# Optimization experiments

Measured on AMD Instinct MI355X. Metric: run time of the kernel, lower is better.

The kernel has to match this reference:

```python
import jax, jax.numpy as jnp
import numpy as np
import math

B, S, D, H, DK, DFF = 64, 512, 512, 8, 64, 2048


def _layernorm(x, g, b, eps=1e-5):
    mu = jnp.mean(x, axis=-1, keepdims=True)
    var = jnp.var(x, axis=-1, keepdims=True)
    return (x - mu) * jax.lax.rsqrt(var + eps) * g + b


def setup_inputs() -> dict:
    key = jax.random.key(0)
    ks = jax.random.split(key, 16)
    std = 0.02
    return {
        "query": jax.random.normal(ks[0], (B, S, D), jnp.float32),
        "key": jax.random.normal(ks[1], (B, S, D), jnp.float32),
        "values": jax.random.normal(ks[2], (B, S, D), jnp.float32),
        "forget_rate": jax.random.uniform(ks[3], (B, 1, S, 1), jnp.float32),
        "Wq": jax.random.normal(ks[4], (D, D), jnp.float32) * std,
        "bq": jnp.zeros((D,), jnp.float32),
        "Wk": jax.random.normal(ks[5], (D, D), jnp.float32) * std,
        "bk": jnp.zeros((D,), jnp.float32),
        "Wv": jax.random.normal(ks[6], (D, D), jnp.float32) * std,
        "bv": jnp.zeros((D,), jnp.float32),
        "Wo": jax.random.normal(ks[7], (D, D), jnp.float32) * std,
        "bo": jnp.zeros((D,), jnp.float32),
        "g1": jnp.ones((D,), jnp.float32),
        "beta1": jnp.zeros((D,), jnp.float32),
        "W1": jax.random.normal(ks[8], (D, DFF), jnp.float32) * std,
        "bf1": jnp.zeros((DFF,), jnp.float32),
        "W2": jax.random.normal(ks[9], (DFF, D), jnp.float32) * std,
        "bf2": jnp.zeros((D,), jnp.float32),
        "g2": jnp.ones((D,), jnp.float32),
        "beta2": jnp.zeros((D,), jnp.float32),
        "mask": 0,
    }


def reference(query, key, values, forget_rate, Wq, bq, Wk, bk, Wv, bv, Wo, bo,
              g1, beta1, W1, bf1, W2, bf2, g2, beta2, mask):
    bs, seqlen, _ = query.shape
    # project and split heads -> [B, H, S, DK]
    q = (query @ Wq + bq).reshape(bs, seqlen, H, DK).transpose(0, 2, 1, 3)
    k = (key @ Wk + bk).reshape(bs, seqlen, H, DK).transpose(0, 2, 1, 3)
    v = (values @ Wv + bv).reshape(bs, seqlen, H, DK).transpose(0, 2, 1, 3)

    scores = jnp.einsum('bhqd,bhkd->bhqk', q, k) / math.sqrt(DK)  # [B,H,S,S]
    # forget_rate [B,1,S,1] broadcasts over heads and key dim (== repeat in torch)
    scores = scores * forget_rate
    # src_mask: allowed where triu(ones, k=mask) == 0, i.e. j < i + mask
    allowed = jnp.tril(jnp.ones((seqlen, seqlen), bool), mask - 1)
    scores = jnp.where(allowed, scores, jnp.float32(-1e32))
    probs = jax.nn.softmax(scores, axis=-1)
    if mask == 0:  # zero_pad: overwrite first query row with zeros
        probs = probs.at[:, :, 0, :].set(0.0)
    out = jnp.einsum('bhqk,bhkd->bhqd', probs, v)  # [B,H,S,DK]
    concat = out.transpose(0, 2, 1, 3).reshape(bs, seqlen, D)
    attn_out = concat @ Wo + bo

    x = _layernorm(query + attn_out, g1, beta1)
    ff = jax.nn.relu(x @ W1 + bf1) @ W2 + bf2
    x = _layernorm(x + ff, g2, beta2)
    return x
```

## Files before the change

kernel.cpp:

```cpp
#include <hip/hip_runtime.h>
#include <hip/hip_bf16.h>
#include <stdint.h>

typedef __attribute__((ext_vector_type(8))) short short8;
typedef __attribute__((ext_vector_type(8))) unsigned short ushort8;
typedef __attribute__((ext_vector_type(4))) unsigned short ushort4v;
typedef __attribute__((ext_vector_type(4))) float f32x4;

#define DEV static __device__ __forceinline__

constexpr int Bc = 64, Sc = 512, Dc = 512, Hc = 8, DKc = 64, DFc = 2048;
constexpr int Mtot = Bc * Sc;
constexpr int CB   = 16;
constexpr int RC   = CB * Sc;

DEV unsigned short f2b(float f) {
    union { float f; unsigned u; } x; x.f = f;
    unsigned r = x.u + 0x7fffu + ((x.u >> 16) & 1u);
    return (unsigned short)(r >> 16);
}
DEV float b2f(unsigned short u) {
    union { unsigned u; float f; } x; x.u = ((unsigned)u) << 16; return x.f;
}

DEV void gload16(const void* g, void* l) {
    __builtin_amdgcn_global_load_lds(
        (const __attribute__((address_space(1))) void*)g,
        (__attribute__((address_space(3))) void*)l, 16, 0, 0);
}

__global__ void k_cvt(const float* __restrict__ in, unsigned short* __restrict__ out, int n8) {
    int idx = blockIdx.x * 256 + threadIdx.x;
    if (idx >= n8) return;
    const float4* p = (const float4*)(in + (size_t)idx * 8);
    float4 a = p[0], b = p[1];
    ushort8 o;
    o[0] = f2b(a.x); o[1] = f2b(a.y); o[2] = f2b(a.z); o[3] = f2b(a.w);
    o[4] = f2b(b.x); o[5] = f2b(b.y); o[6] = f2b(b.z); o[7] = f2b(b.w);
    *(ushort8*)(out + (size_t)idx * 8) = o;
}

__global__ void k_copy8(const unsigned short* __restrict__ in, unsigned short* __restrict__ out, int n8) {
    int idx = blockIdx.x * 256 + threadIdx.x;
    if (idx >= n8) return;
    *(ushort8*)(out + (size_t)idx * 8) = *(const ushort8*)(in + (size_t)idx * 8);
}

__global__ void k_cvt_w_all(
    const float* __restrict__ Wq, const float* __restrict__ Wk, const float* __restrict__ Wv,
    const float* __restrict__ Wo, const float* __restrict__ W1, const float* __restrict__ W2,
    unsigned short* __restrict__ Wqt, unsigned short* __restrict__ Wkt,
    unsigned short* __restrict__ Wvt, unsigned short* __restrict__ Wot,
    unsigned short* __restrict__ W1t, unsigned short* __restrict__ W2t) {
    int idx = blockIdx.x * 256 + threadIdx.x;
    const float* in; unsigned short* out; int K, N, li;
    if (idx < 131072) {
        int w = idx >> 15, r = idx & 32767;
        const float* ins[4] = {Wq, Wk, Wv, Wo};
        unsigned short* outs[4] = {Wqt, Wkt, Wvt, Wot};
        in = ins[w]; out = outs[w]; K = 512; N = 512; li = r;
    } else if (idx < 262144) {
        in = W1; out = W1t; K = 512; N = 2048; li = idx - 131072;
    } else {
        in = W2; out = W2t; K = 2048; N = 512; li = idx - 262144;
    }
    int kc = li % (K / 8), n = li / (K / 8);
    ushort8 o;
    #pragma unroll
    for (int j = 0; j < 8; ++j) o[j] = f2b(in[(size_t)(kc * 8 + j) * N + n]);
    *(ushort8*)(out + (size_t)n * K + kc * 8) = o;
}

__global__ void k_cvt_all(
    const float* __restrict__ Wq, const float* __restrict__ Wk, const float* __restrict__ Wv,
    const float* __restrict__ Wo, const float* __restrict__ W1, const float* __restrict__ W2,
    unsigned short* __restrict__ Wqt, unsigned short* __restrict__ Wkt,
    unsigned short* __restrict__ Wvt, unsigned short* __restrict__ Wot,
    unsigned short* __restrict__ W1t, unsigned short* __restrict__ W2t,
    const float* __restrict__ q_in, const float* __restrict__ k_in, const float* __restrict__ v_in,
    unsigned short* __restrict__ q_out, unsigned short* __restrict__ k_out,
    unsigned short* __restrict__ v_out) {
    int idx = blockIdx.x * 256 + threadIdx.x;
    if (idx >= 393216) {
        int a = idx - 393216;
        const float* in; unsigned short* out; int li;
        if (a < 2097152)       { in = q_in; out = q_out; li = a; }
        else if (a < 4194304)  { in = k_in; out = k_out; li = a - 2097152; }
        else                   { in = v_in; out = v_out; li = a - 4194304; }
        const float4* p = (const float4*)(in + (size_t)li * 8);
        float4 x = p[0], y = p[1];
        ushort8 o;
        o[0] = f2b(x.x); o[1] = f2b(x.y); o[2] = f2b(x.z); o[3] = f2b(x.w);
        o[4] = f2b(y.x); o[5] = f2b(y.y); o[6] = f2b(y.z); o[7] = f2b(y.w);
        *(ushort8*)(out + (size_t)li * 8) = o;
        return;
    }
    const float* in; unsigned short* out; int K, N, li;
    if (idx < 131072) {
        int w = idx >> 15, r = idx & 32767;
        const float* ins[4] = {Wq, Wk, Wv, Wo};
        unsigned short* outs[4] = {Wqt, Wkt, Wvt, Wot};
        in = ins[w]; out = outs[w]; K = 512; N = 512; li = r;
    } else if (idx < 262144) {
        in = W1; out = W1t; K = 512; N = 2048; li = idx - 131072;
    } else {
        in = W2; out = W2t; K = 2048; N = 512; li = idx - 262144;
    }
    int kc = li % (K / 8), n = li / (K / 8);
    ushort8 o;
    #pragma unroll
    for (int j = 0; j < 8; ++j) o[j] = f2b(in[(size_t)(kc * 8 + j) * N + n]);
    *(ushort8*)(out + (size_t)n * K + kc * 8) = o;
}

template<int BM, int BN>
DEV void gemm_core(const unsigned short* __restrict__ A, int lda,
                   const unsigned short* __restrict__ Bt, int ldb, int K,
                   unsigned short* lA, unsigned short* lB,
                   f32x4 (&acc)[BM / 32][BN / 32]) {
    constexpr int MF = BM / 32, NF = BN / 32;
    const int tid = threadIdx.x, lane = tid & 63, wv = tid >> 6;
    const int wr = wv >> 1, wc = wv & 1;
    const int l15 = lane & 15, l4 = lane >> 4, l7 = l15 & 7;
    #pragma unroll
    for (int mf = 0; mf < MF; ++mf)
        #pragma unroll
        for (int nf = 0; nf < NF; ++nf)
            acc[mf][nf] = f32x4{0.f, 0.f, 0.f, 0.f};

    auto stage = [&](int buf, int kt0) {
        unsigned short* dA = lA + (size_t)buf * BM * 64;
        #pragma unroll
        for (int r = 0; r < BM / 32; ++r) {
            int c = r * 256 + tid, row = c >> 3, gs = c & 7;
            gload16(A + (size_t)row * lda + kt0 + ((gs ^ (row & 7)) * 8),
                    dA + (size_t)(r * 256 + wv * 64) * 8);
        }
        unsigned short* dB = lB + (size_t)buf * BN * 64;
        #pragma unroll
        for (int r = 0; r < BN / 32; ++r) {
            int c = r * 256 + tid, row = c >> 3, gs = c & 7;
            gload16(Bt + (size_t)row * ldb + kt0 + ((gs ^ (row & 7)) * 8),
                    dB + (size_t)(r * 256 + wv * 64) * 8);
        }
    };

    stage(0, 0);
    __syncthreads();
    const int nk = K / 64;
    for (int t = 0; t < nk; ++t) {
        const int buf = t & 1;
        if (t + 1 < nk) stage(buf ^ 1, (t + 1) * 64);
        const unsigned short* cA = lA + (size_t)buf * BM * 64;
        const unsigned short* cB = lB + (size_t)buf * BN * 64;
        #pragma unroll
        for (int kt = 0; kt < 2; ++kt) {
            short8 af[MF], bfr[NF];
            #pragma unroll
            for (int mf = 0; mf < MF; ++mf)
                af[mf] = *(const short8*)&cA[(wr * (BM / 2) + mf * 16 + l15) * 64 +
                                             (((kt * 4 + l4) ^ l7) * 8)];
            #pragma unroll
            for (int nf = 0; nf < NF; ++nf)
                bfr[nf] = *(const short8*)&cB[(wc * (BN / 2) + nf * 16 + l15) * 64 +
                                              (((kt * 4 + l4) ^ l7) * 8)];
            #pragma unroll
            for (int mf = 0; mf < MF; ++mf)
                #pragma unroll
                for (int nf = 0; nf < NF; ++nf)
                    acc[mf][nf] = __builtin_amdgcn_mfma_f32_16x16x32_bf16(af[mf], bfr[nf], acc[mf][nf], 0, 0, 0);
        }
        __syncthreads();
    }
}

__global__ __launch_bounds__(256) void k_gemm_qkv(
    const unsigned short* __restrict__ X, const unsigned short* __restrict__ Wt,
    const float* __restrict__ bias, unsigned short* __restrict__ out, int which) {
    __shared__ unsigned short lA[2 * 128 * 64], lB[2 * 128 * 64];
    int m0 = blockIdx.x * 128, n0 = blockIdx.y * 128;
    f32x4 acc[4][4];
    gemm_core<128, 128>(X + (size_t)m0 * Dc, Dc, Wt + (size_t)n0 * Dc, Dc, Dc, lA, lB, acc);
    const int lane = threadIdx.x & 63, wv = threadIdx.x >> 6;
    const int wr = wv >> 1, wc = wv & 1, l15 = lane & 15, l4 = lane >> 4;
    #pragma unroll
    for (int mf = 0; mf < 4; ++mf) {
        #pragma unroll
        for (int nf = 0; nf < 4; ++nf) {
            int n = n0 + wc * 64 + nf * 16 + l15;
            int h = n >> 6, dk = n & 63;
            float bv = bias[n];
            if (which == 2) {
                int mg = m0 + wr * 64 + mf * 16 + l4 * 4;
                int b = mg >> 9, s = mg & 511;
                ushort4v o;
                #pragma unroll
                for (int r = 0; r < 4; ++r) o[r] = f2b(acc[mf][nf][r] + bv);
                *(ushort4v*)&out[((size_t)(b * Hc + h) * DKc + dk) * Sc + s] = o;
            } else {
                float scale = (which == 0) ? 0.125f : 1.0f;
                #pragma unroll
                for (int r = 0; r < 4; ++r) {
                    int mg = m0 + wr * 64 + mf * 16 + l4 * 4 + r;
                    int b = mg >> 9, s = mg & 511;
                    out[((size_t)(b * Hc + h) * Sc + s) * DKc + dk] = f2b((acc[mf][nf][r] + bv) * scale);
                }
            }
        }
    }
}

__global__ __launch_bounds__(256) void k_flash(
    const unsigned short* __restrict__ Qb, const unsigned short* __restrict__ Kb,
    const unsigned short* __restrict__ Vt, unsigned short* __restrict__ conc,
    const float* __restrict__ fr, const int* __restrict__ maskp, int b_base) {
    __shared__ unsigned short lKb[2][64 * 64];
    __shared__ unsigned short lVb[2][64 * 64];
    __shared__ unsigned short lP[128 * 64];
    const int head = blockIdx.y, bl = head >> 3, h = head & 7;
    const int bg = b_base + bl;
    const int m0 = (Sc / 128 - 1 - blockIdx.x) * 128;
    const int mv = *maskp;
    const int tid = threadIdx.x, lane = tid & 63, w = tid >> 6;
    const int l15 = lane & 15, l4 = lane >> 4;
    const int l7 = l15 & 7;
    const int rw = w * 32;
    constexpr float LOG2E = 1.44269504088896340736f;

    unsigned short* lQ = &lKb[0][0];
    const unsigned short* Qg = Qb + ((size_t)head * Sc + m0) * DKc;
    #pragma unroll
    for (int r = 0; r < 4; ++r) {
        int c = r * 256 + tid, row = c >> 3, gs = c & 7;
        gload16(Qg + (size_t)row * DKc + ((gs ^ (row & 7)) * 8), lQ + (size_t)(r * 256 + w * 64) * 8);
    }
    __syncthreads();
    short8 qf[2][2];
    #pragma unroll
    for (int kt = 0; kt < 2; ++kt)
        #pragma unroll
        for (int mf = 0; mf < 2; ++mf)
            qf[kt][mf] = *(const short8*)&lQ[(rw + mf * 16 + l15) * 64 + (((kt * 4 + l4) ^ l7) * 8)];
    float frr[8];
    #pragma unroll
    for (int mf = 0; mf < 2; ++mf)
        #pragma unroll
        for (int r = 0; r < 4; ++r)
            frr[mf * 4 + r] = fr[(size_t)bg * Sc + m0 + rw + mf * 16 + l4 * 4 + r] * LOG2E;
    __syncthreads();

    f32x4 accO[2][4];
    #pragma unroll
    for (int mf = 0; mf < 2; ++mf)
        #pragma unroll
        for (int nf = 0; nf < 4; ++nf)
            accO[mf][nf] = f32x4{0.f, 0.f, 0.f, 0.f};
    float l_run[8];
    #pragma unroll
    for (int i = 0; i < 8; ++i) l_run[i] = 0.f;

    const unsigned short* Kg0 = Kb + (size_t)head * Sc * DKc;
    const unsigned short* Vg0 = Vt + (size_t)head * DKc * Sc;
    int nt = ((m0 + 126 + mv) >> 7) + 1;
    if (nt > 4) nt = 4;
    if (nt < 1) nt = 1;
    const int nc = nt * 2;

    {
        const unsigned short* Kg = Kg0;
        const unsigned short* Vg = Vg0;
        #pragma unroll
        for (int r = 0; r < 2; ++r) {
            int c = r * 256 + tid, row = c >> 3, gs = c & 7;
            gload16(Kg + (size_t)row * DKc + ((gs ^ (row & 7)) * 8), &lKb[0][0] + (size_t)(r * 256 + w * 64) * 8);
            gload16(Vg + (size_t)row * Sc + ((gs ^ (row & 7)) * 8), &lVb[0][0] + (size_t)(r * 256 + w * 64) * 8);
        }
    }
    __syncthreads();

    for (int ci = 0; ci < nc; ++ci) {
        const int buf = ci & 1;
        if (ci + 1 < nc) {
            int n1 = (ci + 1) * 64;
            const unsigned short* Kg = Kg0 + (size_t)n1 * DKc;
            const unsigned short* Vg = Vg0 + n1;
            #pragma unroll
            for (int r = 0; r < 2; ++r) {
                int c = r * 256 + tid, row = c >> 3, gs = c & 7;
                gload16(Kg + (size_t)row * DKc + ((gs ^ (row & 7)) * 8),
                        &lKb[buf ^ 1][0] + (size_t)(r * 256 + w * 64) * 8);
                gload16(Vg + (size_t)row * Sc + ((gs ^ (row & 7)) * 8),
                        &lVb[buf ^ 1][0] + (size_t)(r * 256 + w * 64) * 8);
            }
        }
        const int n0c = ci * 64;
        short8 bk[4][2];
        #pragma unroll
        for (int j = 0; j < 4; ++j)
            #pragma unroll
            for (int kt = 0; kt < 2; ++kt)
                bk[j][kt] = *(const short8*)&lKb[buf][(j * 16 + l15) * 64 + (((kt * 4 + l4) ^ l7) * 8)];
        #pragma unroll
        for (int mf = 0; mf < 2; ++mf) {
            f32x4 sa[4];
            #pragma unroll
            for (int j = 0; j < 4; ++j) sa[j] = f32x4{0.f, 0.f, 0.f, 0.f};
            #pragma unroll
            for (int kt = 0; kt < 2; ++kt)
                #pragma unroll
                for (int j = 0; j < 4; ++j)
                    sa[j] = __builtin_amdgcn_mfma_f32_16x16x32_bf16(qf[kt][mf], bk[j][kt], sa[j], 0, 0, 0);
            #pragma unroll
            for (int r = 0; r < 4; ++r) {
                int rowl = rw + mf * 16 + l4 * 4 + r;
                int rowg = m0 + rowl;
                int prs = rowl & 7;
                float fres = frr[mf * 4 + r];
                float ps = 0.f;
                #pragma unroll
                for (int j = 0; j < 4; ++j) {
                    int colg = n0c + j * 16 + l15;
                    float p = (colg < rowg + mv) ? exp2f(sa[j][r] * fres) : 0.f;
                    ps += p;
                    int gw = j * 2 + (l15 >> 3);
                    lP[rowl * 64 + ((gw ^ prs) * 8) + l7] = f2b(p);
                }
                l_run[mf * 4 + r] += ps;
            }
        }
        #pragma unroll
        for (int kl = 0; kl < 2; ++kl) {
            short8 pa[2];
            #pragma unroll
            for (int mf = 0; mf < 2; ++mf)
                pa[mf] = *(const short8*)&lP[(rw + mf * 16 + l15) * 64 + (((kl * 4 + l4) ^ l7) * 8)];
            #pragma unroll
            for (int nf = 0; nf < 4; ++nf) {
                short8 bv8 = *(const short8*)&lVb[buf][(nf * 16 + l15) * 64 + (((kl * 4 + l4) ^ l7) * 8)];
                #pragma unroll
                for (int mf = 0; mf < 2; ++mf)
                    accO[mf][nf] = __builtin_amdgcn_mfma_f32_16x16x32_bf16(pa[mf], bv8, accO[mf][nf], 0, 0, 0);
            }
        }
        __syncthreads();
    }
    #pragma unroll
    for (int mf = 0; mf < 2; ++mf)
        #pragma unroll
        for (int r = 0; r < 4; ++r) {
            int rowg = m0 + rw + mf * 16 + l4 * 4 + r;
            float l = l_run[mf * 4 + r];
            #pragma unroll
            for (int o = 1; o < 16; o <<= 1) l += __shfl_xor(l, o);
            float inv = (rowg + mv > 0) ? 1.0f / l : 0.f;
            #pragma unroll
            for (int nf = 0; nf < 4; ++nf) {
                int dk = nf * 16 + l15;
                conc[((size_t)bg * Sc + rowg) * Dc + h * DKc + dk] = f2b(accO[mf][nf][r] * inv);
            }
        }
}

__global__ __launch_bounds__(256) void k_wo(
    const unsigned short* __restrict__ Cc, const unsigned short* __restrict__ Wot,
    const float* __restrict__ bo, const float* __restrict__ query, float* __restrict__ y) {
    __shared__ unsigned short lA[2 * 128 * 64], lB[2 * 128 * 64];
    int m0 = blockIdx.x * 128, n0 = blockIdx.y * 128;
    f32x4 acc[4][4];
    gemm_core<128, 128>(Cc + (size_t)m0 * Dc, Dc, Wot + (size_t)n0 * Dc, Dc, Dc, lA, lB, acc);
    const int lane = threadIdx.x & 63, wv = threadIdx.x >> 6;
    const int wr = wv >> 1, wc = wv & 1, l15 = lane & 15, l4 = lane >> 4;
    #pragma unroll
    for (int mf = 0; mf < 4; ++mf)
        #pragma unroll
        for (int nf = 0; nf < 4; ++nf) {
            int n = n0 + wc * 64 + nf * 16 + l15;
            float bv = bo[n];
            #pragma unroll
            for (int r = 0; r < 4; ++r) {
                int m = m0 + wr * 64 + mf * 16 + l4 * 4 + r;
                y[(size_t)m * Dc + n] = acc[mf][nf][r] + bv + query[(size_t)m * Dc + n];
            }
        }
}

__global__ __launch_bounds__(256) void k_ff1(
    const unsigned short* __restrict__ X, const unsigned short* __restrict__ W1t,
    const float* __restrict__ b1, unsigned short* __restrict__ hb) {
    __shared__ unsigned short lA[2 * 128 * 64], lB[2 * 128 * 64];
    int m0 = blockIdx.x * 128, n0 = blockIdx.y * 128;
    f32x4 acc[4][4];
    gemm_core<128, 128>(X + (size_t)m0 * Dc, Dc, W1t + (size_t)n0 * Dc, Dc, Dc, lA, lB, acc);
    const int lane = threadIdx.x & 63, wv = threadIdx.x >> 6;
    const int wr = wv >> 1, wc = wv & 1, l15 = lane & 15, l4 = lane >> 4;
    #pragma unroll
    for (int mf = 0; mf < 4; ++mf)
        #pragma unroll
        for (int nf = 0; nf < 4; ++nf) {
            int n = n0 + wc * 64 + nf * 16 + l15;
            float bv = b1[n];
            #pragma unroll
            for (int r = 0; r < 4; ++r) {
                int m = m0 + wr * 64 + mf * 16 + l4 * 4 + r;
                hb[(size_t)m * DFc + n] = f2b(fmaxf(acc[mf][nf][r] + bv, 0.f));
            }
        }
}

__global__ __launch_bounds__(256) void k_ff2b(
    const unsigned short* __restrict__ Hb, const unsigned short* __restrict__ W2t,
    const float* __restrict__ b2, const unsigned short* __restrict__ residb,
    float* __restrict__ y) {
    __shared__ unsigned short lA[2 * 128 * 64], lB[2 * 128 * 64];
    int m0 = blockIdx.x * 128, n0 = blockIdx.y * 128;
    f32x4 acc[4][4];
    gemm_core<128, 128>(Hb + (size_t)m0 * DFc, DFc, W2t + (size_t)n0 * DFc, DFc, DFc, lA, lB, acc);
    const int lane = threadIdx.x & 63, wv = threadIdx.x >> 6;
    const int wr = wv >> 1, wc = wv & 1, l15 = lane & 15, l4 = lane >> 4;
    #pragma unroll
    for (int mf = 0; mf < 4; ++mf)
        #pragma unroll
        for (int nf = 0; nf < 4; ++nf) {
            int n = n0 + wc * 64 + nf * 16 + l15;
            float bv = b2[n];
            #pragma unroll
            for (int r = 0; r < 4; ++r) {
                int m = m0 + wr * 64 + mf * 16 + l4 * 4 + r;
                y[(size_t)m * Dc + n] = acc[mf][nf][r] + bv + b2f(residb[(size_t)m * Dc + n]);
            }
        }
}

__global__ __launch_bounds__(256) void k_ln(
    const float* __restrict__ in, const float* __restrict__ g, const float* __restrict__ be,
    float* __restrict__ outf, unsigned short* __restrict__ outb) {
    int rid = blockIdx.x * 4 + (threadIdx.x >> 6);
    int lane = threadIdx.x & 63;
    const float* row = in + (size_t)rid * Dc;
    float4 a = ((const float4*)row)[lane * 2];
    float4 b = ((const float4*)row)[lane * 2 + 1];
    float x[8] = {a.x, a.y, a.z, a.w, b.x, b.y, b.z, b.w};
    float s = 0.f, ss = 0.f;
    #pragma unroll
    for (int j = 0; j < 8; ++j) { s += x[j]; ss += x[j] * x[j]; }
    #pragma unroll
    for (int o = 1; o < 64; o <<= 1) { s += __shfl_xor(s, o); ss += __shfl_xor(ss, o); }
    float mu = s * (1.f / 512.f);
    float var = ss * (1.f / 512.f) - mu * mu;
    float rs = rsqrtf(var + 1e-5f);
    float4 g0 = ((const float4*)g)[lane * 2], g1v = ((const float4*)g)[lane * 2 + 1];
    float4 e0 = ((const float4*)be)[lane * 2], e1 = ((const float4*)be)[lane * 2 + 1];
    float gg[8] = {g0.x, g0.y, g0.z, g0.w, g1v.x, g1v.y, g1v.z, g1v.w};
    float ee[8] = {e0.x, e0.y, e0.z, e0.w, e1.x, e1.y, e1.z, e1.w};
    float o8[8];
    #pragma unroll
    for (int j = 0; j < 8; ++j) o8[j] = (x[j] - mu) * rs * gg[j] + ee[j];
    if (outf) {
        float4* po = (float4*)(outf + (size_t)rid * Dc);
        float4 w0 = {o8[0], o8[1], o8[2], o8[3]}, w1 = {o8[4], o8[5], o8[6], o8[7]};
        po[lane * 2] = w0; po[lane * 2 + 1] = w1;
    }
    if (outb) {
        ushort8 ob;
        #pragma unroll
        for (int j = 0; j < 8; ++j) ob[j] = f2b(o8[j]);
        *(ushort8*)(outb + (size_t)rid * Dc + lane * 8) = ob;
    }
}

extern "C" void kernel_launch(void* const* d_in, const int* in_sizes, int n_in,
                              void* d_out, int out_size, void* d_ws, size_t ws_size,
                              hipStream_t stream) {
    const float* query = (const float*)d_in[0];
    const float* key_  = (const float*)d_in[1];
    const float* vals  = (const float*)d_in[2];
    const float* fr    = (const float*)d_in[3];
    const float* Wq = (const float*)d_in[4];  const float* bq = (const float*)d_in[5];
    const float* Wk = (const float*)d_in[6];  const float* bk = (const float*)d_in[7];
    const float* Wv = (const float*)d_in[8];  const float* bv = (const float*)d_in[9];
    const float* Wo = (const float*)d_in[10]; const float* bo = (const float*)d_in[11];
    const float* g1 = (const float*)d_in[12]; const float* be1 = (const float*)d_in[13];
    const float* W1 = (const float*)d_in[14]; const float* b1 = (const float*)d_in[15];
    const float* W2 = (const float*)d_in[16]; const float* b2 = (const float*)d_in[17];
    const float* g2 = (const float*)d_in[18]; const float* be2 = (const float*)d_in[19];
    const int* maskp = (const int*)d_in[20];
    float* out = (float*)d_out;

    char* ab = (char*)d_out;
    unsigned short* xb    = (unsigned short*)ab;
    unsigned short* conc  = (unsigned short*)ab;
    unsigned short* x1b   = conc;
    unsigned short* keyst = (unsigned short*)(ab + (size_t)32 * 1048576);
    unsigned short* Qc   = (unsigned short*)(ab + (size_t)32 * 1048576);
    unsigned short* Kc   = (unsigned short*)(ab + (size_t)40 * 1048576);
    unsigned short* Vc   = (unsigned short*)(ab + (size_t)48 * 1048576);
    unsigned short* xst  = (unsigned short*)(ab + (size_t)56 * 1048576);
    float*          xfc  = (float*)(ab + (size_t)32 * 1048576);

    char* ws = (char*)d_ws;
    unsigned short* Wqt = (unsigned short*)ws;
    unsigned short* Wkt = Wqt + 512 * 512;
    unsigned short* Wvt = Wkt + 512 * 512;
    unsigned short* Wot = Wvt + 512 * 512;
    unsigned short* W1t = Wot + 512 * 512;
    unsigned short* W2t = W1t + 2048 * 512;
    char* wend = (char*)(W2t + 512 * 2048);
    size_t wrem = (ws_size > (size_t)(wend - ws)) ? ws_size - (size_t)(wend - ws) : 0;
    const size_t qkvb = (size_t)Mtot * Dc * 2;

    const bool bigpath = (wrem >= 3 * qkvb);

    const float* acts[3] = {query, key_, vals};
    const unsigned short* wt3[3] = {Wqt, Wkt, Wvt};
    const float* bs3[3] = {bq, bk, bv};

    if (bigpath) {
        unsigned short* QbF = (unsigned short*)wend;
        unsigned short* KbF = QbF + qkvb / 2;
        unsigned short* VtF = KbF + qkvb / 2;
        unsigned short* hb     = QbF;
        unsigned short* resid0 = VtF;
        float*          xf     = (float*)KbF;
        const int Mc = 16384;

        k_cvt_all<<<dim3(26112), dim3(256), 0, stream>>>(
            Wq, Wk, Wv, Wo, W1, W2, Wqt, Wkt, Wvt, Wot, W1t, W2t,
            query, key_, vals, xb, keyst, KbF);

        k_gemm_qkv<<<dim3(Mtot / 128, 4), dim3(256), 0, stream>>>(KbF,   Wvt, bv, VtF, 2);
        k_gemm_qkv<<<dim3(Mtot / 128, 4), dim3(256), 0, stream>>>(keyst, Wkt, bk, KbF, 1);
        k_gemm_qkv<<<dim3(Mtot / 128, 4), dim3(256), 0, stream>>>(xb,    Wqt, bq, QbF, 0);

        k_flash<<<dim3(Sc / 128, Bc * Hc), dim3(256), 0, stream>>>(QbF, KbF, VtF, conc, fr, maskp, 0);

        k_wo<<<dim3(Mtot / 128, 4), dim3(256), 0, stream>>>(conc, Wot, bo, query, xf);
        k_ln<<<dim3(Mtot / 4), dim3(256), 0, stream>>>(xf, g1, be1, (float*)nullptr, x1b);

        k_copy8<<<dim3(Mc / 4), dim3(256), 0, stream>>>(x1b, resid0, Mc * Dc / 8);

        for (int mb = Mtot - Mc; mb >= 0; mb -= Mc) {
            k_ff1<<<dim3(Mc / 128, 16), dim3(256), 0, stream>>>(x1b + (size_t)mb * Dc, W1t, b1, hb);
            k_ff2b<<<dim3(Mc / 128, 4), dim3(256), 0, stream>>>(hb, W2t, b2,
                                                                mb ? x1b + (size_t)mb * Dc : resid0,
                                                                out + (size_t)mb * Dc);
            k_ln<<<dim3(Mc / 4), dim3(256), 0, stream>>>(out + (size_t)mb * Dc, g2, be2,
                                                         out + (size_t)mb * Dc, (unsigned short*)nullptr);
        }
    } else {
        int Mc = 128;
        for (int c = 8192; c >= 128; c >>= 1)
            if ((size_t)c * 5120 <= wrem) { Mc = c; break; }
        unsigned short* hb     = (unsigned short*)wend;
        unsigned short* resid0 = (unsigned short*)(wend + (size_t)Mc * 4096);

        k_cvt_w_all<<<dim3(1536), dim3(256), 0, stream>>>(Wq, Wk, Wv, Wo, W1, W2,
                                                          Wqt, Wkt, Wvt, Wot, W1t, W2t);
        unsigned short* out3[3] = {Qc, Kc, Vc};
        for (int cb = 0; cb < Bc / CB; ++cb) {
            for (int p = 0; p < 3; ++p) {
                k_cvt<<<dim3(RC * Dc / 8 / 256), dim3(256), 0, stream>>>(
                    acts[p] + (size_t)cb * RC * Dc, xst, RC * Dc / 8);
                k_gemm_qkv<<<dim3(RC / 128, 4), dim3(256), 0, stream>>>(xst, wt3[p], bs3[p], out3[p], p);
            }
            k_flash<<<dim3(Sc / 128, CB * Hc), dim3(256), 0, stream>>>(Qc, Kc, Vc, conc, fr, maskp, cb * CB);
        }
        for (int hp = 0; hp < 2; ++hp) {
            int mb = hp * 16384;
            k_wo<<<dim3(16384 / 128, 4), dim3(256), 0, stream>>>(conc + (size_t)mb * Dc, Wot, bo,
                                                                 query + (size_t)mb * Dc, xfc);
            k_ln<<<dim3(16384 / 4), dim3(256), 0, stream>>>(xfc, g1, be1, (float*)nullptr,
                                                            x1b + (size_t)mb * Dc);
        }
        k_copy8<<<dim3(Mc / 4), dim3(256), 0, stream>>>(x1b, resid0, Mc * Dc / 8);
        for (int mb = Mtot - Mc; mb >= 0; mb -= Mc) {
            k_ff1<<<dim3(Mc / 128, 16), dim3(256), 0, stream>>>(x1b + (size_t)mb * Dc, W1t, b1, hb);
            k_ff2b<<<dim3(Mc / 128, 4), dim3(256), 0, stream>>>(hb, W2t, b2,
                                                                mb ? x1b + (size_t)mb * Dc : resid0,
                                                                out + (size_t)mb * Dc);
            k_ln<<<dim3(Mc / 4), dim3(256), 0, stream>>>(out + (size_t)mb * Dc, g2, be2,
                                                         out + (size_t)mb * Dc, (unsigned short*)nullptr);
        }
    }
}
```

Baseline: 579.5 us.

## Enlarge flash attention query tile to 256 rows with 512-thread blocks

The flash kernel now handles 256 query rows per block with 8 waves instead of 128 rows with 4 waves, and shared memory is merged into one buffer. Each K/V chunk loaded into LDS is shared by twice as many query rows, which halves global K/V traffic and block count. The cost is coarser causal work skipping, since the diagonal tile is larger and the number of chunks is set per 256-row block. It also lowers the block count and may reduce occupancy through the larger LDS footprint and 512-thread launch bound.

```diff
diff --git a/kernel.cpp b/kernel.cpp
--- a/kernel.cpp
+++ b/kernel.cpp
@@ -210,29 +210,28 @@
     }
 }
 
-__global__ __launch_bounds__(256) void k_flash(
+__global__ __launch_bounds__(512) void k_flash(
     const unsigned short* __restrict__ Qb, const unsigned short* __restrict__ Kb,
     const unsigned short* __restrict__ Vt, unsigned short* __restrict__ conc,
     const float* __restrict__ fr, const int* __restrict__ maskp, int b_base) {
-    __shared__ unsigned short lKb[2][64 * 64];
-    __shared__ unsigned short lVb[2][64 * 64];
-    __shared__ unsigned short lP[128 * 64];
+    __shared__ unsigned short smem[32768];
     const int head = blockIdx.y, bl = head >> 3, h = head & 7;
     const int bg = b_base + bl;
-    const int m0 = (Sc / 128 - 1 - blockIdx.x) * 128;
+    const int m0 = (Sc / 256 - 1 - blockIdx.x) * 256;
     const int mv = *maskp;
     const int tid = threadIdx.x, lane = tid & 63, w = tid >> 6;
     const int l15 = lane & 15, l4 = lane >> 4;
     const int l7 = l15 & 7;
     const int rw = w * 32;
+    unsigned short* lP = smem + 16384;
     constexpr float LOG2E = 1.44269504088896340736f;
 
-    unsigned short* lQ = &lKb[0][0];
+    unsigned short* lQ = smem;
     const unsigned short* Qg = Qb + ((size_t)head * Sc + m0) * DKc;
     #pragma unroll
     for (int r = 0; r < 4; ++r) {
-        int c = r * 256 + tid, row = c >> 3, gs = c & 7;
-        gload16(Qg + (size_t)row * DKc + ((gs ^ (row & 7)) * 8), lQ + (size_t)(r * 256 + w * 64) * 8);
+        int c = r * 512 + tid, row = c >> 3, gs = c & 7;
+        gload16(Qg + (size_t)row * DKc + ((gs ^ (row & 7)) * 8), lQ + (size_t)(r * 512 + w * 64) * 8);
     }
     __syncthreads();
     short8 qf[2][2];
@@ -261,37 +260,28 @@
 
     const unsigned short* Kg0 = Kb + (size_t)head * Sc * DKc;
     const unsigned short* Vg0 = Vt + (size_t)head * DKc * Sc;
-    int nt = ((m0 + 126 + mv) >> 7) + 1;
-    if (nt > 4) nt = 4;
-    if (nt < 1) nt = 1;
-    const int nc = nt * 2;
+    int nc = ((m0 + 254 + mv) >> 6) + 1;
+    if (nc > 8) nc = 8;
+    if (nc < 1) nc = 1;
 
     {
-        const unsigned short* Kg = Kg0;
-        const unsigned short* Vg = Vg0;
-        #pragma unroll
-        for (int r = 0; r < 2; ++r) {
-            int c = r * 256 + tid, row = c >> 3, gs = c & 7;
-            gload16(Kg + (size_t)row * DKc + ((gs ^ (row & 7)) * 8), &lKb[0][0] + (size_t)(r * 256 + w * 64) * 8);
-            gload16(Vg + (size_t)row * Sc + ((gs ^ (row & 7)) * 8), &lVb[0][0] + (size_t)(r * 256 + w * 64) * 8);
-        }
+        int row = tid >> 3, gs = tid & 7;
+        gload16(Kg0 + (size_t)row * DKc + ((gs ^ (row & 7)) * 8), smem + (size_t)(w * 64) * 8);
+        gload16(Vg0 + (size_t)row * Sc + ((gs ^ (row & 7)) * 8), smem + 8192 + (size_t)(w * 64) * 8);
     }
     __syncthreads();
 
     for (int ci = 0; ci < nc; ++ci) {
         const int buf = ci & 1;
+        unsigned short* lK = smem + (size_t)buf * 4096;
+        unsigned short* lV = smem + 8192 + (size_t)buf * 4096;
         if (ci + 1 < nc) {
             int n1 = (ci + 1) * 64;
-            const unsigned short* Kg = Kg0 + (size_t)n1 * DKc;
-            const unsigned short* Vg = Vg0 + n1;
-            #pragma unroll
-            for (int r = 0; r < 2; ++r) {
-                int c = r * 256 + tid, row = c >> 3, gs = c & 7;
-                gload16(Kg + (size_t)row * DKc + ((gs ^ (row & 7)) * 8),
-                        &lKb[buf ^ 1][0] + (size_t)(r * 256 + w * 64) * 8);
-                gload16(Vg + (size_t)row * Sc + ((gs ^ (row & 7)) * 8),
-                        &lVb[buf ^ 1][0] + (size_t)(r * 256 + w * 64) * 8);
-            }
+            int row = tid >> 3, gs = tid & 7;
+            gload16(Kg0 + (size_t)n1 * DKc + (size_t)row * DKc + ((gs ^ (row & 7)) * 8),
+                    smem + (size_t)(buf ^ 1) * 4096 + (size_t)(w * 64) * 8);
+            gload16(Vg0 + n1 + (size_t)row * Sc + ((gs ^ (row & 7)) * 8),
+                    smem + 8192 + (size_t)(buf ^ 1) * 4096 + (size_t)(w * 64) * 8);
         }
         const int n0c = ci * 64;
         short8 bk[4][2];
@@ -299,7 +289,7 @@
         for (int j = 0; j < 4; ++j)
             #pragma unroll
             for (int kt = 0; kt < 2; ++kt)
-                bk[j][kt] = *(const short8*)&lKb[buf][(j * 16 + l15) * 64 + (((kt * 4 + l4) ^ l7) * 8)];
+                bk[j][kt] = *(const short8*)&lK[(j * 16 + l15) * 64 + (((kt * 4 + l4) ^ l7) * 8)];
         #pragma unroll
         for (int mf = 0; mf < 2; ++mf) {
             f32x4 sa[4];
@@ -336,7 +326,7 @@
                 pa[mf] = *(const short8*)&lP[(rw + mf * 16 + l15) * 64 + (((kl * 4 + l4) ^ l7) * 8)];
             #pragma unroll
             for (int nf = 0; nf < 4; ++nf) {
-                short8 bv8 = *(const short8*)&lVb[buf][(nf * 16 + l15) * 64 + (((kl * 4 + l4) ^ l7) * 8)];
+                short8 bv8 = *(const short8*)&lV[(nf * 16 + l15) * 64 + (((kl * 4 + l4) ^ l7) * 8)];
                 #pragma unroll
                 for (int mf = 0; mf < 2; ++mf)
                     accO[mf][nf] = __builtin_amdgcn_mfma_f32_16x16x32_bf16(pa[mf], bv8, accO[mf][nf], 0, 0, 0);
@@ -531,7 +521,7 @@
         k_gemm_qkv<<<dim3(Mtot / 128, 4), dim3(256), 0, stream>>>(keyst, Wkt, bk, KbF, 1);
         k_gemm_qkv<<<dim3(Mtot / 128, 4), dim3(256), 0, stream>>>(xb,    Wqt, bq, QbF, 0);
 
-        k_flash<<<dim3(Sc / 128, Bc * Hc), dim3(256), 0, stream>>>(QbF, KbF, VtF, conc, fr, maskp, 0);
+        k_flash<<<dim3(Sc / 256, Bc * Hc), dim3(512), 0, stream>>>(QbF, KbF, VtF, conc, fr, maskp, 0);
 
         k_wo<<<dim3(Mtot / 128, 4), dim3(256), 0, stream>>>(conc, Wot, bo, query, xf);
         k_ln<<<dim3(Mtot / 4), dim3(256), 0, stream>>>(xf, g1, be1, (float*)nullptr, x1b);
@@ -562,7 +552,7 @@
                     acts[p] + (size_t)cb * RC * Dc, xst, RC * Dc / 8);
                 k_gemm_qkv<<<dim3(RC / 128, 4), dim3(256), 0, stream>>>(xst, wt3[p], bs3[p], out3[p], p);
             }
-            k_flash<<<dim3(Sc / 128, CB * Hc), dim3(256), 0, stream>>>(Qc, Kc, Vc, conc, fr, maskp, cb * CB);
+            k_flash<<<dim3(Sc / 256, CB * Hc), dim3(512), 0, stream>>>(Qc, Kc, Vc, conc, fr, maskp, cb * CB);
         }
         for (int hp = 0; hp < 2; ++hp) {
             int mb = hp * 16384;
```

After: 563.9 us. 1.03x faster.
